# Optimization experiments

Hardware: AMD Instinct MI355X
Metric: run time of the kernel (lower is better)

The kernel has to match this reference:

```python
import jax, jax.numpy as jnp
import numpy as np

HIDDEN = 1024
HEADS = 16
HEAD_DIM = HIDDEN // HEADS


def setup_inputs() -> dict:
    key = jax.random.key(0)
    ks = jax.random.split(key, 10)
    B, S, D = 4, 2048, HIDDEN
    scale = 1.0 / np.sqrt(D)
    x = jax.random.normal(ks[0], (B, S, D), dtype=jnp.float32)
    mask = jax.random.bernoulli(ks[1], 0.1, (B, S))  # True = masked position
    Wq = jax.random.normal(ks[2], (D, D), dtype=jnp.float32) * scale
    Wk = jax.random.normal(ks[3], (D, D), dtype=jnp.float32) * scale
    Wv = jax.random.normal(ks[4], (D, D), dtype=jnp.float32) * scale
    Wo = jax.random.normal(ks[5], (D, D), dtype=jnp.float32) * scale
    bq = jnp.zeros((D,), jnp.float32)
    bk = jnp.zeros((D,), jnp.float32)
    bv = jnp.zeros((D,), jnp.float32)
    bo = jnp.zeros((D,), jnp.float32)
    return {"x": x, "mask": mask, "Wq": Wq, "bq": bq, "Wk": Wk, "bk": bk,
            "Wv": Wv, "bv": bv, "Wo": Wo, "bo": bo}


def reference(x, mask, Wq, bq, Wk, bk, Wv, bv, Wo, bo):
    B, S, D = x.shape
    H, dh = HEADS, HEAD_DIM
    # QKV projections -> [B, H, S, dh]
    def proj(W, b):
        return (x @ W + b).reshape(B, S, H, dh).transpose(0, 2, 1, 3)
    q, k, v = proj(Wq, bq), proj(Wk, bk), proj(Wv, bv)
    # scaled dot-product scores [B, H, S, S]
    scores = jnp.einsum("bhqd,bhkd->bhqk", q, k) / jnp.sqrt(jnp.asarray(dh, x.dtype))
    neg = jnp.finfo(x.dtype).min
    scores = jnp.where(mask[:, None, None, :], neg, scores)
    attn = jax.nn.softmax(scores, axis=-1)
    out = jnp.einsum("bhqk,bhkd->bhqd", attn, v)  # [B, H, S, dh]
    out = out.transpose(0, 2, 1, 3).reshape(B, S, D)
    return out @ Wo + bo  # dropout p=0.0 -> identity
```

## Files before the change

kernel.cpp:

```cpp
#include <hip/hip_runtime.h>
#include <hip/hip_bf16.h>

typedef __attribute__((ext_vector_type(8))) short bf8_t;
typedef __attribute__((ext_vector_type(4))) float f4_t;
typedef __attribute__((ext_vector_type(2))) unsigned int u2_t;
typedef __attribute__((ext_vector_type(4))) unsigned int u4_t;

#define MFMA16(a, b, c) __builtin_amdgcn_mfma_f32_16x16x32_bf16((a), (b), (c), 0, 0, 0)

static __device__ inline unsigned short f2bf(float f) {
    unsigned int u = __float_as_uint(f);
    unsigned int r = 0x7fffu + ((u >> 16) & 1u);
    return (unsigned short)((u + r) >> 16);
}

static __device__ inline float exp2_fast(float x) {
    float r;
    asm("v_exp_f32 %0, %1" : "=v"(r) : "v"(x));
    return r;
}

static __device__ inline unsigned int cvtpk_bf16(float lo, float hi) {
    unsigned int r;
    asm("v_cvt_pk_bf16_f32 %0, %1, %2" : "=v"(r) : "v"(lo), "v"(hi));
    return r;
}

static __device__ inline void gload16(const void* g, void* l) {
    __builtin_amdgcn_global_load_lds(
        (const __attribute__((address_space(1))) unsigned int*)g,
        (__attribute__((address_space(3))) unsigned int*)l, 16, 0, 0);
}

__global__ void k_bias(const void* __restrict__ maskp, float* __restrict__ fbias) {
    __shared__ int s_int, s_flt;
    const unsigned int* mw = (const unsigned int*)maskp;
    if (threadIdx.x == 0) { s_int = 1; s_flt = 1; }
    __syncthreads();
    int li = 1, lf = 1;
    for (int i = threadIdx.x; i < 2048; i += 1024) {
        unsigned int v = mw[i];
        if (v != 0u && v != 1u) li = 0;
        if (v != 0u && v != 0x3F800000u) lf = 0;
    }
    if (!li) atomicAnd(&s_int, 0);
    if (!lf) atomicAnd(&s_flt, 0);
    __syncthreads();
    const int flag = s_int ? 0 : (s_flt ? 1 : 2);
    const int*           mi = (const int*)maskp;
    const float*         mf = (const float*)maskp;
    const unsigned char* mb = (const unsigned char*)maskp;
    for (int i = threadIdx.x; i < 8192; i += 1024) {
        bool m = (flag == 0) ? (mi[i] != 0) : (flag == 1) ? (mf[i] != 0.0f) : (mb[i] != 0);
        fbias[i] = m ? -1e30f : 0.0f;
    }
}

__global__ void k_cvt(const float* __restrict__ x, unsigned short* __restrict__ xb, int n4) {
    int i = blockIdx.x * blockDim.x + threadIdx.x;
    if (i < n4) {
        float4 v = ((const float4*)x)[i];
        ushort4 o;
        o.x = f2bf(v.x); o.y = f2bf(v.y); o.z = f2bf(v.z); o.w = f2bf(v.w);
        ((ushort4*)xb)[i] = o;
    }
}

__global__ void k_transw(const float* __restrict__ Wq, const float* __restrict__ Wk,
                         const float* __restrict__ Wv, const float* __restrict__ Wo,
                         unsigned short* __restrict__ WT) {
    __shared__ float tile[32][33];
    const float* W = (blockIdx.z == 0) ? Wq : (blockIdx.z == 1) ? Wk : (blockIdx.z == 2) ? Wv : Wo;
    unsigned short* out = WT + (size_t)blockIdx.z * 1024 * 1024;
    int n_r = blockIdx.x * 32 + threadIdx.x;
    int k_r = blockIdx.y * 32 + threadIdx.y;
    #pragma unroll
    for (int j = 0; j < 32; j += 8)
        tile[threadIdx.y + j][threadIdx.x] = W[(size_t)(k_r + j) * 1024 + n_r];
    __syncthreads();
    int k_w = blockIdx.y * 32 + threadIdx.x;
    int n_w = blockIdx.x * 32 + threadIdx.y;
    #pragma unroll
    for (int j = 0; j < 32; j += 8)
        out[(size_t)(n_w + j) * 1024 + k_w] = f2bf(tile[threadIdx.x][threadIdx.y + j]);
}

template <int MODE>
__global__ __launch_bounds__(256) void k_gemm(
    const unsigned short* __restrict__ A,
    const unsigned short* __restrict__ WTb,
    const float* __restrict__ b0, const float* __restrict__ b1, const float* __restrict__ b2,
    void* __restrict__ outp, void* __restrict__ outp2)
{
    __shared__ __align__(16) unsigned short SH[17408];
    auto Als = (unsigned short (*)[128][32])(SH);
    auto Bls = (unsigned short (*)[128][32])(SH + 8192);
    const int tid  = threadIdx.x;
    const int lane = tid & 63;
    const int w    = tid >> 6;
    const int wr   = w >> 1, wc = w & 1;
    const int lg   = lane >> 4, lr = lane & 15;
    const int lg4  = lg * 4;

    const int id   = blockIdx.x;
    const int xcd  = id & 7;
    const int j    = id >> 3;
    const int ncol = j >> 3;
    const int by   = xcd * 8 + (j & 7);
    const int z    = (MODE == 0) ? (ncol >> 3) : 0;
    const int bm   = by * 128;
    const int bn   = ((MODE == 0) ? (ncol & 7) : ncol) * 128;
    const unsigned short* WT = WTb + (MODE == 0 ? (size_t)z * (1024 * 1024) : 0);

    f4_t acc[4][4];
    const f4_t z4 = {0.f, 0.f, 0.f, 0.f};
    #pragma unroll
    for (int i = 0; i < 4; ++i)
        #pragma unroll
        for (int jj = 0; jj < 4; ++jj) acc[i][jj] = z4;

    int strow[2], stcol[2];
    #pragma unroll
    for (int p = 0; p < 2; ++p) {
        int o = p * 4096 + tid * 16;
        strow[p] = o >> 6;
        stcol[p] = o & 63;
    }

    auto stage = [&](int buf, int k0) {
        #pragma unroll
        for (int p = 0; p < 2; ++p) {
            int o = p * 4096 + tid * 16;
            gload16((const char*)(A  + (size_t)(bm + strow[p]) * 1024 + k0) + stcol[p],
                    (char*)&Als[buf][0][0] + o);
            gload16((const char*)(WT + (size_t)(bn + strow[p]) * 1024 + k0) + stcol[p],
                    (char*)&Bls[buf][0][0] + o);
        }
    };

    stage(0, 0);
    __syncthreads();

    for (int k0 = 0; k0 < 1024; k0 += 32) {
        const int buf = (k0 >> 5) & 1;
        if (k0 + 32 < 1024) stage(buf ^ 1, k0 + 32);

        bf8_t af[4], bfv[4];
        #pragma unroll
        for (int i = 0; i < 4; ++i) af[i]  = *(const bf8_t*)(&Als[buf][wr * 64 + i * 16 + lr][lg * 8]);
        #pragma unroll
        for (int jj = 0; jj < 4; ++jj) bfv[jj] = *(const bf8_t*)(&Bls[buf][wc * 64 + jj * 16 + lr][lg * 8]);
        __builtin_amdgcn_s_setprio(1);
        #pragma unroll
        for (int i = 0; i < 4; ++i)
            #pragma unroll
            for (int jj = 0; jj < 4; ++jj)
                acc[i][jj] = MFMA16(af[i], bfv[jj], acc[i][jj]);
        __builtin_amdgcn_s_setprio(0);

        __syncthreads();
    }

    if (MODE == 0) {
        const float* bias = (z == 0) ? b0 : (z == 1) ? b1 : b2;
        const float sc = (z == 0) ? 0.18033688011112042f : 1.0f;
        const int bb = bm >> 11;
        const int sb = bm & 2047;

        if (z < 2) {
            #pragma unroll
            for (int i = 0; i < 4; ++i)
                #pragma unroll
                for (int jj = 0; jj < 4; ++jj) {
                    int c = wc * 64 + jj * 16 + lr;
                    float bcol = bias[bn + c];
                    #pragma unroll
                    for (int r = 0; r < 4; ++r) {
                        int s = wr * 64 + i * 16 + lg4 + r;
                        SH[s * 136 + c] = f2bf((acc[i][jj][r] + bcol) * sc);
                    }
                }
            __syncthreads();
            unsigned short* O = (unsigned short*)outp + (size_t)z * (8192 * 1024);
            #pragma unroll
            for (int it = 0; it < 8; ++it) {
                int idx = it * 256 + tid;
                int hh  = idx >> 10;
                int rem = idx & 1023;
                int ss  = rem >> 3;
                int cc  = rem & 7;
                u4_t v = *(const u4_t*)&SH[ss * 136 + hh * 64 + cc * 8];
                int hq = (bn >> 6) + hh;
                *(u4_t*)(O + (((size_t)(bb * 16 + hq)) * 2048 + sb + ss) * 64 + cc * 8) = v;
            }
        } else {
            #pragma unroll
            for (int i = 0; i < 4; ++i) {
                int spb = wr * 64 + 32 * (i >> 1) + 8 * lg + 4 * (i & 1);
                #pragma unroll
                for (int jj = 0; jj < 4; ++jj) {
                    int c = wc * 64 + jj * 16 + lr;
                    float bcol = bias[bn + c];
                    #pragma unroll
                    for (int r = 0; r < 4; ++r)
                        SH[c * 136 + spb + r] = f2bf(acc[i][jj][r] + bcol);
                }
            }
            __syncthreads();
            unsigned short* OT = (unsigned short*)outp2;
            #pragma unroll
            for (int it = 0; it < 8; ++it) {
                int idx  = it * 256 + tid;
                int drow = idx >> 4;
                int cc   = idx & 15;
                u4_t v = *(const u4_t*)&SH[drow * 136 + cc * 8];
                int dcol = bn + drow;
                int hq = dcol >> 6, dh = dcol & 63;
                *(u4_t*)(OT + (((size_t)(bb * 16 + hq)) * 64 + dh) * 2048 + sb + cc * 8) = v;
            }
        }
    } else {
        float* O = (float*)outp;
        float* SF = (float*)SH;
        #pragma unroll
        for (int hhalf = 0; hhalf < 2; ++hhalf) {
            if (wr == hhalf) {
                #pragma unroll
                for (int i = 0; i < 4; ++i)
                    #pragma unroll
                    for (int jj = 0; jj < 4; ++jj) {
                        int c = wc * 64 + jj * 16 + lr;
                        float bcol = b0[bn + c];
                        #pragma unroll
                        for (int r = 0; r < 4; ++r)
                            SF[(i * 16 + lg4 + r) * 132 + c] = acc[i][jj][r] + bcol;
                    }
            }
            __syncthreads();
            #pragma unroll
            for (int it = 0; it < 8; ++it) {
                int idx = it * 256 + tid;
                int ss  = idx >> 5;
                int cc  = idx & 31;
                u4_t v = *(const u4_t*)&SF[ss * 132 + cc * 4];
                *(u4_t*)(O + (size_t)(bm + hhalf * 64 + ss) * 1024 + bn + cc * 4) = v;
            }
            __syncthreads();
        }
    }
}

__global__ __launch_bounds__(256, 2) void k_attn(
    const unsigned short* __restrict__ Q,
    const unsigned short* __restrict__ K,
    const unsigned short* __restrict__ VT,
    const float* __restrict__ fbias,
    unsigned short* __restrict__ O)
{
    __shared__ __align__(16) unsigned short Kls[2][64][64];
    __shared__ __align__(16) unsigned short Vls[2][64][64];
    const int tid  = threadIdx.x;
    const int lane = tid & 63;
    const int w    = tid >> 6;
    const int lg   = lane >> 4, lr = lane & 15;
    const int lg4  = lg * 4;

    const int id = blockIdx.x;
    const int bh = (id & 7) * 8 + ((id >> 3) & 7);
    const int qt = id >> 6;
    const int b  = bh >> 4, h = bh & 15;
    const int q0 = qt * 256 + w * 64;
    const size_t base = (size_t)bh * (2048 * 64);

    const char* Kbase = (const char*)(K + base);
    const char* Vbase = (const char*)(VT + (size_t)bh * (64 * 2048));

    int srow[2], scol[2];
    #pragma unroll
    for (int p = 0; p < 2; ++p) {
        int o = p * 4096 + tid * 16;
        srow[p] = o >> 7;
        scol[p] = (o & 127) ^ ((srow[p] & 7) << 4);
    }

    auto stage = [&](int buf, int k0) {
        #pragma unroll
        for (int p = 0; p < 2; ++p) {
            int o = p * 4096 + tid * 16;
            gload16(Kbase + (size_t)(k0 + srow[p]) * 128 + scol[p],
                    (char*)&Kls[buf][0][0] + o);
            gload16(Vbase + (size_t)srow[p] * 4096 + (size_t)k0 * 2 + scol[p],
                    (char*)&Vls[buf][0][0] + o);
        }
    };

    bf8_t qf[4][2];
    #pragma unroll
    for (int sub = 0; sub < 4; ++sub) {
        const unsigned short* qp = Q + base + (size_t)(q0 + sub * 16 + lr) * 64 + lg * 8;
        qf[sub][0] = *(const bf8_t*)qp;
        qf[sub][1] = *(const bf8_t*)(qp + 32);
    }

    const f4_t z4 = {0.f, 0.f, 0.f, 0.f};
    f4_t oacc[4][4];
    #pragma unroll
    for (int sub = 0; sub < 4; ++sub)
        #pragma unroll
        for (int nf = 0; nf < 4; ++nf) oacc[sub][nf] = z4;
    f4_t lacc[4] = {z4, z4, z4, z4};

    u4_t uones = {0x3F803F80u, 0x3F803F80u, 0x3F803F80u, 0x3F803F80u};
    const bf8_t ones8 = __builtin_bit_cast(bf8_t, uones);

    const float* fb = fbias + b * 2048 + lg4;
    const int sw = (lr & 7) << 4;
    const int cA = (lg * 16) ^ sw;
    const int cB = (64 + lg * 16) ^ sw;
    const int vA = (16 * lg) ^ sw;
    const int vB = (64 + 16 * lg) ^ sw;

    auto sm = [&](f4_t (&s)[4], u4_t (&pf)[2]) {
        #pragma unroll
        for (int c2 = 0; c2 < 2; ++c2) {
            float e0 = exp2_fast(s[2*c2][0]);
            float e1 = exp2_fast(s[2*c2][1]);
            float e2 = exp2_fast(s[2*c2][2]);
            float e3 = exp2_fast(s[2*c2][3]);
            float e4 = exp2_fast(s[2*c2+1][0]);
            float e5 = exp2_fast(s[2*c2+1][1]);
            float e6 = exp2_fast(s[2*c2+1][2]);
            float e7 = exp2_fast(s[2*c2+1][3]);
            u4_t u;
            u.x = cvtpk_bf16(e0, e1);
            u.y = cvtpk_bf16(e2, e3);
            u.z = cvtpk_bf16(e4, e5);
            u.w = cvtpk_bf16(e6, e7);
            pf[c2] = u;
        }
    };

    auto tile_body = [&](int cur, int k0) {
        f4_t cb[4];
        #pragma unroll
        for (int mf = 0; mf < 4; ++mf)
            cb[mf] = *(const f4_t*)(fb + k0 + mf * 16);

        bf8_t kf[4][2];
        #pragma unroll
        for (int mf = 0; mf < 4; ++mf) {
            const char* kr = (const char*)&Kls[cur][mf * 16 + lr][0];
            kf[mf][0] = *(const bf8_t*)(kr + cA);
            kf[mf][1] = *(const bf8_t*)(kr + cB);
        }
        bf8_t vf[4][2];
        #pragma unroll
        for (int nf = 0; nf < 4; ++nf) {
            const char* vr = (const char*)&Vls[cur][nf * 16 + lr][0];
            vf[nf][0] = *(const bf8_t*)(vr + vA);
            vf[nf][1] = *(const bf8_t*)(vr + vB);
        }

        #pragma unroll
        for (int sub = 0; sub < 4; ++sub) {
            f4_t s[4];
            __builtin_amdgcn_s_setprio(1);
            #pragma unroll
            for (int mf = 0; mf < 4; ++mf)
                s[mf] = MFMA16(kf[mf][1], qf[sub][1], MFMA16(kf[mf][0], qf[sub][0], cb[mf]));
            __builtin_amdgcn_s_setprio(0);

            u4_t pf[2];
            sm(s, pf);

            __builtin_amdgcn_s_setprio(1);
            #pragma unroll
            for (int c = 0; c < 2; ++c) {
                bf8_t pb = __builtin_bit_cast(bf8_t, pf[c]);
                lacc[sub] = MFMA16(ones8, pb, lacc[sub]);
                #pragma unroll
                for (int nf = 0; nf < 4; ++nf)
                    oacc[sub][nf] = MFMA16(vf[nf][c], pb, oacc[sub][nf]);
            }
            __builtin_amdgcn_s_setprio(0);
        }
    };

    stage(0, 0);
    __syncthreads();

    #pragma unroll 1
    for (int tt = 0; tt < 16; ++tt) {
        stage(1, (2 * tt + 1) * 64);
        tile_body(0, 2 * tt * 64);
        __syncthreads();
        if (tt < 15) stage(0, (2 * tt + 2) * 64);
        tile_body(1, (2 * tt + 1) * 64);
        __syncthreads();
    }

    #pragma unroll
    for (int sub = 0; sub < 4; ++sub) {
        float inv = 1.0f / lacc[sub][0];
        int qrow = q0 + sub * 16 + lr;
        size_t ob = ((size_t)(b * 2048 + qrow)) * 1024 + h * 64 + lg4;
        #pragma unroll
        for (int nf = 0; nf < 4; ++nf) {
            u2_t uo;
            uo.x = cvtpk_bf16(oacc[sub][nf][0] * inv, oacc[sub][nf][1] * inv);
            uo.y = cvtpk_bf16(oacc[sub][nf][2] * inv, oacc[sub][nf][3] * inv);
            *(u2_t*)(O + ob + nf * 16) = uo;
        }
    }
}

extern "C" void kernel_launch(void* const* d_in, const int* in_sizes, int n_in,
                              void* d_out, int out_size, void* d_ws, size_t ws_size,
                              hipStream_t stream) {
    const float* x  = (const float*)d_in[0];
    const void*  mask = d_in[1];
    const float* Wq = (const float*)d_in[2];
    const float* bq = (const float*)d_in[3];
    const float* Wk = (const float*)d_in[4];
    const float* bk = (const float*)d_in[5];
    const float* Wv = (const float*)d_in[6];
    const float* bv = (const float*)d_in[7];
    const float* Wo = (const float*)d_in[8];
    const float* bo = (const float*)d_in[9];

    char* ws = (char*)d_ws;
    float*          fbias = (float*)(ws + 1024);
    unsigned short* xb    = (unsigned short*)(ws + 65536);
    unsigned short* wT    = (unsigned short*)(ws + 65536 + 16777216);
    unsigned short* qkv   = (unsigned short*)(ws + 65536 + 25165824);
    unsigned short* attnb = (unsigned short*)(ws + 65536 + 75497472);

    unsigned short* Qb = qkv;
    unsigned short* Kb = qkv + 8388608;
    unsigned short* VT = qkv + 16777216;

    k_bias<<<1, 1024, 0, stream>>>(mask, fbias);
    k_cvt<<<8192, 256, 0, stream>>>(x, xb, 2097152);
    k_transw<<<dim3(32, 32, 4), dim3(32, 8), 0, stream>>>(Wq, Wk, Wv, Wo, wT);
    k_gemm<0><<<1536, 256, 0, stream>>>(xb, wT, bq, bk, bv, (void*)qkv, (void*)VT);
    k_attn<<<512, 256, 0, stream>>>(Qb, Kb, VT, fbias, attnb);
    k_gemm<1><<<512, 256, 0, stream>>>(attnb, wT + 3145728, bo, bo, bo, d_out, nullptr);
}
```

Before: 169.9 us.

## Triple-buffer GEMM K-loop with explicit vmcnt waits and raw barriers

Changes the projection GEMM's shared-memory staging from double to triple buffering, so each K step prefetches two tiles ahead. It uses explicit s_waitcnt vmcnt counts and raw s_barrier calls with sched_barrier fences in place of one __syncthreads per iteration. The goal is to hide global-to-LDS load latency behind the MFMA work. In exchange, LDS use rises from 34 KB to 48 KB per block, which may cut occupancy, and correctness now depends on the hand-counted outstanding load numbers.

Measured after the change: 183.3 us. +7.9%, slower.

```diff
diff --git a/kernel.cpp b/kernel.cpp
--- a/kernel.cpp
+++ b/kernel.cpp
@@ -92,9 +92,7 @@
     const float* __restrict__ b0, const float* __restrict__ b1, const float* __restrict__ b2,
     void* __restrict__ outp, void* __restrict__ outp2)
 {
-    __shared__ __align__(16) unsigned short SH[17408];
-    auto Als = (unsigned short (*)[128][32])(SH);
-    auto Bls = (unsigned short (*)[128][32])(SH + 8192);
+    __shared__ __align__(16) unsigned short SH[24576];
     const int tid  = threadIdx.x;
     const int lane = tid & 63;
     const int w    = tid >> 6;
@@ -127,29 +125,23 @@
         stcol[p] = o & 63;
     }
 
-    auto stage = [&](int buf, int k0) {
+    auto stage = [&](char* base, int k0) {
         #pragma unroll
         for (int p = 0; p < 2; ++p) {
             int o = p * 4096 + tid * 16;
-            gload16((const char*)(A  + (size_t)(bm + strow[p]) * 1024 + k0) + stcol[p],
-                    (char*)&Als[buf][0][0] + o);
-            gload16((const char*)(WT + (size_t)(bn + strow[p]) * 1024 + k0) + stcol[p],
-                    (char*)&Bls[buf][0][0] + o);
+            gload16((const char*)(A  + (size_t)(bm + strow[p]) * 1024 + k0) + stcol[p], base + o);
+            gload16((const char*)(WT + (size_t)(bn + strow[p]) * 1024 + k0) + stcol[p], base + 8192 + o);
         }
     };
 
-    stage(0, 0);
-    __syncthreads();
-
-    for (int k0 = 0; k0 < 1024; k0 += 32) {
-        const int buf = (k0 >> 5) & 1;
-        if (k0 + 32 < 1024) stage(buf ^ 1, k0 + 32);
-
+    auto compute = [&](const char* base) {
         bf8_t af[4], bfv[4];
         #pragma unroll
-        for (int i = 0; i < 4; ++i) af[i]  = *(const bf8_t*)(&Als[buf][wr * 64 + i * 16 + lr][lg * 8]);
-        #pragma unroll
-        for (int jj = 0; jj < 4; ++jj) bfv[jj] = *(const bf8_t*)(&Bls[buf][wc * 64 + jj * 16 + lr][lg * 8]);
+        for (int i = 0; i < 4; ++i)
+            af[i]  = *(const bf8_t*)(base + (wr * 64 + i * 16 + lr) * 64 + lg * 16);
+        #pragma unroll
+        for (int jj = 0; jj < 4; ++jj)
+            bfv[jj] = *(const bf8_t*)(base + 8192 + (wc * 64 + jj * 16 + lr) * 64 + lg * 16);
         __builtin_amdgcn_s_setprio(1);
         #pragma unroll
         for (int i = 0; i < 4; ++i)
@@ -157,9 +149,38 @@
             for (int jj = 0; jj < 4; ++jj)
                 acc[i][jj] = MFMA16(af[i], bfv[jj], acc[i][jj]);
         __builtin_amdgcn_s_setprio(0);
-
-        __syncthreads();
-    }
+    };
+
+    char* cur = (char*)SH;
+    char* nxt = (char*)SH + 16384;
+    char* fut = (char*)SH + 32768;
+
+    stage(cur, 0);
+    stage(nxt, 32);
+
+    #pragma unroll 1
+    for (int t = 0; t < 30; ++t) {
+        stage(fut, (t + 2) * 32);
+        asm volatile("s_waitcnt vmcnt(8)" ::: "memory");
+        __builtin_amdgcn_s_barrier();
+        __builtin_amdgcn_sched_barrier(0);
+        compute(cur);
+        __builtin_amdgcn_s_barrier();
+        __builtin_amdgcn_sched_barrier(0);
+        char* tmp = cur; cur = nxt; nxt = fut; fut = tmp;
+    }
+    asm volatile("s_waitcnt vmcnt(4)" ::: "memory");
+    __builtin_amdgcn_s_barrier();
+    __builtin_amdgcn_sched_barrier(0);
+    compute(cur);
+    __builtin_amdgcn_s_barrier();
+    __builtin_amdgcn_sched_barrier(0);
+    { char* tmp = cur; cur = nxt; nxt = fut; fut = tmp; }
+    asm volatile("s_waitcnt vmcnt(0)" ::: "memory");
+    __builtin_amdgcn_s_barrier();
+    __builtin_amdgcn_sched_barrier(0);
+    compute(cur);
+    __syncthreads();
 
     if (MODE == 0) {
         const float* bias = (z == 0) ? b0 : (z == 1) ? b1 : b2;
```

## Deepen GEMM K-tile to 64 with XOR-swizzled LDS and unrolled double buffer

Applied to the files above, without the earlier changes.

The projection GEMM's K step grows from 32 to 64 elements per stage, with each LDS buffer 128x64 per operand (64KB total). Staging writes and fragment reads use an XOR swizzle on the 16-byte column to avoid LDS bank conflicts. The main loop is manually unrolled across the two buffers, which halves the number of barriers per K. In exchange, LDS use rises to 64KB per block, which may reduce occupancy, and register pressure goes up from the doubled fragment arrays.

Measured after the change: 163.9 us. 1.04x faster.

```diff
diff --git a/kernel.cpp b/kernel.cpp
--- a/kernel.cpp
+++ b/kernel.cpp
@@ -92,9 +92,7 @@
     const float* __restrict__ b0, const float* __restrict__ b1, const float* __restrict__ b2,
     void* __restrict__ outp, void* __restrict__ outp2)
 {
-    __shared__ __align__(16) unsigned short SH[17408];
-    auto Als = (unsigned short (*)[128][32])(SH);
-    auto Bls = (unsigned short (*)[128][32])(SH + 8192);
+    __shared__ __align__(16) unsigned short SH[32768];
     const int tid  = threadIdx.x;
     const int lane = tid & 63;
     const int w    = tid >> 6;
@@ -119,45 +117,59 @@
         #pragma unroll
         for (int jj = 0; jj < 4; ++jj) acc[i][jj] = z4;
 
-    int strow[2], stcol[2];
-    #pragma unroll
-    for (int p = 0; p < 2; ++p) {
+    int strow[4], stcol[4];
+    #pragma unroll
+    for (int p = 0; p < 4; ++p) {
         int o = p * 4096 + tid * 16;
-        strow[p] = o >> 6;
-        stcol[p] = o & 63;
+        strow[p] = o >> 7;
+        stcol[p] = (o & 127) ^ ((strow[p] & 7) << 4);
     }
 
     auto stage = [&](int buf, int k0) {
-        #pragma unroll
-        for (int p = 0; p < 2; ++p) {
+        char* base = (char*)SH + buf * 32768;
+        #pragma unroll
+        for (int p = 0; p < 4; ++p) {
             int o = p * 4096 + tid * 16;
-            gload16((const char*)(A  + (size_t)(bm + strow[p]) * 1024 + k0) + stcol[p],
-                    (char*)&Als[buf][0][0] + o);
-            gload16((const char*)(WT + (size_t)(bn + strow[p]) * 1024 + k0) + stcol[p],
-                    (char*)&Bls[buf][0][0] + o);
-        }
+            gload16((const char*)(A  + (size_t)(bm + strow[p]) * 1024 + k0) + stcol[p], base + o);
+            gload16((const char*)(WT + (size_t)(bn + strow[p]) * 1024 + k0) + stcol[p], base + 16384 + o);
+        }
+    };
+
+    const int swz = (lr & 7) << 4;
+    auto compute = [&](int buf) {
+        const char* base = (const char*)SH + buf * 32768;
+        bf8_t af[2][4], bfv[2][4];
+        #pragma unroll
+        for (int kk = 0; kk < 2; ++kk) {
+            int col = (kk * 64 + lg * 16) ^ swz;
+            #pragma unroll
+            for (int i = 0; i < 4; ++i)
+                af[kk][i] = *(const bf8_t*)(base + (wr * 64 + i * 16 + lr) * 128 + col);
+            #pragma unroll
+            for (int jj = 0; jj < 4; ++jj)
+                bfv[kk][jj] = *(const bf8_t*)(base + 16384 + (wc * 64 + jj * 16 + lr) * 128 + col);
+        }
+        __builtin_amdgcn_s_setprio(1);
+        #pragma unroll
+        for (int kk = 0; kk < 2; ++kk)
+            #pragma unroll
+            for (int i = 0; i < 4; ++i)
+                #pragma unroll
+                for (int jj = 0; jj < 4; ++jj)
+                    acc[i][jj] = MFMA16(af[kk][i], bfv[kk][jj], acc[i][jj]);
+        __builtin_amdgcn_s_setprio(0);
     };
 
     stage(0, 0);
     __syncthreads();
 
-    for (int k0 = 0; k0 < 1024; k0 += 32) {
-        const int buf = (k0 >> 5) & 1;
-        if (k0 + 32 < 1024) stage(buf ^ 1, k0 + 32);
-
-        bf8_t af[4], bfv[4];
-        #pragma unroll
-        for (int i = 0; i < 4; ++i) af[i]  = *(const bf8_t*)(&Als[buf][wr * 64 + i * 16 + lr][lg * 8]);
-        #pragma unroll
-        for (int jj = 0; jj < 4; ++jj) bfv[jj] = *(const bf8_t*)(&Bls[buf][wc * 64 + jj * 16 + lr][lg * 8]);
-        __builtin_amdgcn_s_setprio(1);
-        #pragma unroll
-        for (int i = 0; i < 4; ++i)
-            #pragma unroll
-            for (int jj = 0; jj < 4; ++jj)
-                acc[i][jj] = MFMA16(af[i], bfv[jj], acc[i][jj]);
-        __builtin_amdgcn_s_setprio(0);
-
+    #pragma unroll 1
+    for (int tt = 0; tt < 8; ++tt) {
+        stage(1, (2 * tt + 1) * 64);
+        compute(0);
+        __syncthreads();
+        if (tt < 7) stage(0, (2 * tt + 2) * 64);
+        compute(1);
         __syncthreads();
     }
 
```
